# Performance work log

Measured on AMD Instinct MI355X. Metric: run time of the kernel, lower is better.

Reference implementation:

```python
import jax, jax.numpy as jnp
import numpy as np

HIDDEN = 2048
HEADS = 16
HEAD = HIDDEN // HEADS  # 128
MB = 16                 # TTT mini-batch size
LR = 1.0                # inner (test-time) learning rate
ROPE_BASE = 10000.0
LN_EPS = 1e-5


def setup_inputs() -> dict:
    key = jax.random.key(0)
    ks = jax.random.split(key, 7)
    B, S = 4, 2048
    scale = HIDDEN ** -0.5
    x = jax.random.normal(ks[0], (B, S, HIDDEN), jnp.float32)
    Wk = jax.random.normal(ks[1], (HIDDEN, HIDDEN), jnp.float32) * scale
    Wv = jax.random.normal(ks[2], (HIDDEN, HIDDEN), jnp.float32) * scale
    Wo = jax.random.normal(ks[3], (HIDDEN, HIDDEN), jnp.float32) * scale
    ln_g = jnp.ones((HIDDEN,), jnp.float32)
    ln_b = jnp.zeros((HIDDEN,), jnp.float32)
    # initial TTT hidden-state weights, per (batch, head)
    W0 = jax.random.normal(ks[4], (B, HEADS, HEAD, HEAD), jnp.float32) * 0.02
    return {"x": x, "Wk": Wk, "Wv": Wv, "Wo": Wo, "ln_g": ln_g, "ln_b": ln_b, "W0": W0}


def _rotate_half(u):
    u1, u2 = jnp.split(u, 2, axis=-1)
    return jnp.concatenate([-u2, u1], axis=-1)


def _rope(k, seq_len):
    # k: [B, H, S, D]
    inv_freq = 1.0 / (ROPE_BASE ** (jnp.arange(0, HEAD, 2, dtype=jnp.float32) / HEAD))
    t = jnp.arange(seq_len, dtype=jnp.float32)
    freqs = t[:, None] * inv_freq[None, :]          # [S, D/2]
    emb = jnp.concatenate([freqs, freqs], axis=-1)  # [S, D]
    cos, sin = jnp.cos(emb), jnp.sin(emb)
    return k * cos[None, None] + _rotate_half(k) * sin[None, None]


def reference(x, Wk, Wv, Wo, ln_g, ln_b, W0):
    B, S, _ = x.shape
    # projections (nn.Linear convention: y = x @ W.T), split into heads
    k = (x @ Wk.T).reshape(B, S, HEADS, HEAD).transpose(0, 2, 1, 3)  # [B,H,S,D]
    v = (x @ Wv.T).reshape(B, S, HEADS, HEAD).transpose(0, 2, 1, 3)
    k = _rope(k, S)

    nc = S // MB
    # [nc, B, H, MB, D]
    kc = k.reshape(B, HEADS, nc, MB, HEAD).transpose(2, 0, 1, 3, 4)
    vc = v.reshape(B, HEADS, nc, MB, HEAD).transpose(2, 0, 1, 3, 4)

    def step(W, kv):
        k_c, v_c = kv                                   # [B,H,MB,D]
        pred = jnp.einsum('bhmd,bhde->bhme', k_c, W)    # f(k; W) = k W
        err = pred - v_c
        # grad of mean-MSE over (MB*D) elements w.r.t. W: 2/(MB*D) * k^T err
        grad = (2.0 / (MB * HEAD)) * jnp.einsum('bhmd,bhme->bhde', k_c, err)
        W_new = W - LR * grad                           # inner SGD step
        out = jnp.einsum('bhmd,bhde->bhme', k_c, W_new) # output with updated weights
        return W_new, out

    W_final, outs = jax.lax.scan(step, W0, (kc, vc))    # outs: [nc,B,H,MB,D]
    o = outs.transpose(1, 2, 0, 3, 4).reshape(B, HEADS, S, HEAD)
    o = o.transpose(0, 2, 1, 3).reshape(B, S, HIDDEN)

    # LayerNorm + output projection + residual
    mu = o.mean(-1, keepdims=True)
    var = o.var(-1, keepdims=True)
    o = (o - mu) / jnp.sqrt(var + LN_EPS) * ln_g + ln_b
    return x + o @ Wo.T
```

## Files before the change

kernel.cpp:

```cpp
#include <hip/hip_runtime.h>
#include <cstdint>
#include <cstddef>

typedef __attribute__((ext_vector_type(4))) float    f32x4;
typedef __attribute__((ext_vector_type(8))) __bf16   bf16x8;
typedef __attribute__((ext_vector_type(4))) short    s16x4;
typedef __attribute__((ext_vector_type(4))) uint32_t u32x4;
typedef __attribute__((ext_vector_type(2))) uint32_t u32x2;

__device__ __forceinline__ float bf2f(uint16_t h) {
    uint32_t u = ((uint32_t)h) << 16;
    return __builtin_bit_cast(float, u);
}
__device__ __forceinline__ uint16_t f2bf(float f) {
    uint32_t u = __builtin_bit_cast(uint32_t, f);
    uint32_t r = (u + 0x7fffu + ((u >> 16) & 1u)) >> 16;
    return (uint16_t)r;
}
__device__ __forceinline__ uint16_t f2bf_fast(float f) {
    __bf16 h = (__bf16)f;
    return __builtin_bit_cast(uint16_t, h);
}

__device__ __forceinline__ f32x4 mfma32(bf16x8 a, bf16x8 b, f32x4 c) {
    return __builtin_amdgcn_mfma_f32_16x16x32_bf16(a, b, c, 0, 0, 0);
}
__device__ __forceinline__ f32x4 mfma16(s16x4 a, s16x4 b, f32x4 c) {
    return __builtin_amdgcn_mfma_f32_16x16x16bf16_1k(a, b, c, 0, 0, 0);
}

__device__ __forceinline__ void gload16(const void* g, void* l) {
    __builtin_amdgcn_global_load_lds(
        (const __attribute__((address_space(1))) uint32_t*)g,
        (__attribute__((address_space(3))) uint32_t*)l, 16, 0, 0);
}

__global__ __launch_bounds__(256) void cvt_bf16(
    const float* __restrict__ s, uint16_t* __restrict__ d, int n4)
{
    int i = blockIdx.x * 256 + threadIdx.x;
    const int stride = gridDim.x * 256;
    for (; i < n4; i += stride) {
        f32x4 v = ((const f32x4*)s)[i];
        u32x2 p;
        p[0] = (uint32_t)f2bf(v[0]) | ((uint32_t)f2bf(v[1]) << 16);
        p[1] = (uint32_t)f2bf(v[2]) | ((uint32_t)f2bf(v[3]) << 16);
        ((u32x2*)d)[i] = p;
    }
}

template <bool F32OUT>
__global__ __launch_bounds__(512, 2) void gemm256(
    const uint16_t* __restrict__ A, const uint16_t* __restrict__ B,
    void* __restrict__ Cv, const float* __restrict__ R,
    int M, int N, int K)
{
    __shared__ __align__(16) uint16_t lA[2][256 * 64];
    __shared__ __align__(16) uint16_t lB[2][256 * 64];

    const int tid = threadIdx.x;
    const int w = tid >> 6, ln = tid & 63;
    const int l15 = ln & 15, q = ln >> 4;
    const int wm = w >> 2, wn = w & 3;
    const int m0 = blockIdx.y * 256, n0 = blockIdx.x * 256;

    const int srow = w * 32 + (ln >> 3);
    const int scol = ((ln & 7) ^ (ln >> 3)) * 8;
    const uint16_t* gA = A + (size_t)(m0 + srow) * K + scol;
    const uint16_t* gB = B + (size_t)(n0 + srow) * K + scol;

    f32x4 acc[8][4];
    #pragma unroll
    for (int i = 0; i < 8; i++)
        for (int j = 0; j < 4; j++)
            acc[i][j] = (f32x4){0.f, 0.f, 0.f, 0.f};

    const int xs  = (l15 & 7) * 8;
    const int aro = (wm * 128 + l15) * 64;
    const int bro = (wn * 64 + l15) * 64;
    const int k0o = (q * 8) ^ xs;
    const int k1o = (32 + q * 8) ^ xs;

    auto stage = [&](int t) {
        const int s = t & 1;
        const int kt = t * 64;
        #pragma unroll
        for (int i = 0; i < 4; i++)
            gload16(gA + (size_t)(i * 8) * K + kt, lA[s] + (w * 32 + i * 8) * 64);
        #pragma unroll
        for (int i = 0; i < 4; i++)
            gload16(gB + (size_t)(i * 8) * K + kt, lB[s] + (w * 32 + i * 8) * 64);
    };

    const int ntk = K >> 6;
    stage(0);
    __syncthreads();

    for (int t = 0; t < ntk; ++t) {
        const int s = t & 1;
        if (t + 1 < ntk) stage(t + 1);

        const uint16_t* As = lA[s];
        const uint16_t* Bs = lB[s];

        bf16x8 a0[8], b0[4];
        #pragma unroll
        for (int mt = 0; mt < 8; mt++)
            a0[mt] = __builtin_bit_cast(bf16x8,
                *(const u32x4*)(As + aro + mt * 1024 + k0o));
        #pragma unroll
        for (int nt2 = 0; nt2 < 4; nt2++)
            b0[nt2] = __builtin_bit_cast(bf16x8,
                *(const u32x4*)(Bs + bro + nt2 * 1024 + k0o));
        #pragma unroll
        for (int mt = 0; mt < 8; mt++)
            #pragma unroll
            for (int nt2 = 0; nt2 < 4; nt2++)
                acc[mt][nt2] = mfma32(a0[mt], b0[nt2], acc[mt][nt2]);

        bf16x8 a1[8], b1[4];
        #pragma unroll
        for (int mt = 0; mt < 8; mt++)
            a1[mt] = __builtin_bit_cast(bf16x8,
                *(const u32x4*)(As + aro + mt * 1024 + k1o));
        #pragma unroll
        for (int nt2 = 0; nt2 < 4; nt2++)
            b1[nt2] = __builtin_bit_cast(bf16x8,
                *(const u32x4*)(Bs + bro + nt2 * 1024 + k1o));
        #pragma unroll
        for (int mt = 0; mt < 8; mt++)
            #pragma unroll
            for (int nt2 = 0; nt2 < 4; nt2++)
                acc[mt][nt2] = mfma32(a1[mt], b1[nt2], acc[mt][nt2]);

        __syncthreads();
    }

    #pragma unroll
    for (int mt = 0; mt < 8; mt++)
        #pragma unroll
        for (int nt2 = 0; nt2 < 4; nt2++)
            #pragma unroll
            for (int r = 0; r < 4; r++) {
                int row = m0 + wm * 128 + mt * 16 + q * 4 + r;
                int col = n0 + wn * 64 + nt2 * 16 + l15;
                size_t idx = (size_t)row * N + col;
                float v = acc[mt][nt2][r];
                if (F32OUT) {
                    ((float*)Cv)[idx] = v + R[idx];
                } else {
                    ((uint16_t*)Cv)[idx] = f2bf(v);
                }
            }
}

__global__ __launch_bounds__(64) void repack(
    const uint16_t* __restrict__ kb, const uint16_t* __restrict__ vb,
    uint16_t* __restrict__ kp, uint16_t* __restrict__ kt,
    uint16_t* __restrict__ vt)
{
    const int g = blockIdx.x;
    const int c = g & 127, h = (g >> 7) & 15, b = g >> 11;
    const int ln = threadIdx.x;
    const int m = ln >> 2, cb = (ln & 3) * 32;
    const size_t tok = (size_t)b * 2048 + c * 16 + m;
    const int s = c * 16 + m;
    const uint16_t* krow = kb + tok * 2048 + h * 128;
    const uint16_t* vrow = vb + tok * 2048 + h * 128;

    u32x4 kraw[4], praw[4], vraw[4];
    for (int i = 0; i < 4; i++) {
        kraw[i] = *(const u32x4*)(krow + cb + 8 * i);
        praw[i] = *(const u32x4*)(krow + (cb ^ 64) + 8 * i);
        vraw[i] = *(const u32x4*)(vrow + cb + 8 * i);
    }
    const uint16_t* ku = (const uint16_t*)kraw;
    const uint16_t* pu = (const uint16_t*)praw;
    const uint16_t* vu = (const uint16_t*)vraw;

    uint16_t ko[32];
    for (int j = 0; j < 32; j++) {
        int col = cb + j;
        int p = col & 63;
        float invf = exp2f((float)p * (-13.287712379549449f / 64.0f));
        float a = (float)s * invf;
        float sn, cs;
        __sincosf(a, &sn, &cs);
        float u1 = bf2f(ku[j]), u2 = bf2f(pu[j]);
        float o = (col < 64) ? (u1 * cs - u2 * sn) : (u1 * cs + u2 * sn);
        ko[j] = f2bf(o);
    }

    uint16_t* kpg = kp + (size_t)g * 2048;
    uint16_t* ktg = kt + (size_t)g * 2048;
    uint16_t* vtg = vt + (size_t)g * 2048;
    for (int i = 0; i < 4; i++) {
        u32x4 pk;
        uint32_t* pw = (uint32_t*)&pk;
        for (int w = 0; w < 4; w++)
            pw[w] = (uint32_t)ko[8 * i + 2 * w] | ((uint32_t)ko[8 * i + 2 * w + 1] << 16);
        *(u32x4*)(kpg + m * 128 + cb + 8 * i) = pk;
    }
    for (int j = 0; j < 32; j++) {
        ktg[(cb + j) * 16 + m] = ko[j];
        vtg[(cb + j) * 16 + m] = vu[j];
    }
}

__global__ __launch_bounds__(64, 1) void ttt_scan(
    const uint16_t* __restrict__ kp, const uint16_t* __restrict__ kt,
    const uint16_t* __restrict__ vt, const float* __restrict__ W0,
    uint16_t* __restrict__ O)
{
    const int bid = blockIdx.x;
    const int g  = bid & 63;
    const int e0 = (bid >> 6) * 16;
    const int h = g & 15, b = g >> 4;
    const int ln = threadIdx.x;
    const int l15 = ln & 15, q = ln >> 4;

    f32x4 W[8];
    s16x4 Wb[8];
    {
        const float* w0p = W0 + (size_t)g * 128 * 128;
        #pragma unroll
        for (int mt = 0; mt < 8; mt++)
            for (int r = 0; r < 4; r++)
                W[mt][r] = w0p[(size_t)(16 * mt + 4 * q + r) * 128 + e0 + l15];
    }
    #pragma unroll
    for (int mt = 0; mt < 8; mt++)
        for (int r = 0; r < 4; r++)
            Wb[mt][r] = (short)f2bf_fast(W[mt][r]);

    const uint16_t* kpw = kp + (size_t)g * 128 * 2048;
    const uint16_t* ktw = kt + (size_t)g * 128 * 2048;
    const uint16_t* vtw = vt + (size_t)g * 128 * 2048;
    uint16_t*     obase = O  + (size_t)b * 2048 * 2048 + h * 128 + e0;

    auto loadset = [&](int c, u32x2* ka, u32x2* ktf, u32x2* vv) {
        const uint16_t* kc = kpw + (size_t)c * 2048;
        const uint16_t* tc = ktw + (size_t)c * 2048;
        const uint16_t* vc = vtw + (size_t)c * 2048;
        #pragma unroll
        for (int dt = 0; dt < 8; dt++)
            ka[dt] = *(const u32x2*)(kc + l15 * 128 + 16 * dt + 4 * q);
        #pragma unroll
        for (int mt = 0; mt < 8; mt++)
            ktf[mt] = *(const u32x2*)(tc + (16 * mt + l15) * 16 + 4 * q);
        vv[0] = *(const u32x2*)(vc + (e0 + l15) * 16 + 4 * q);
    };

    auto step = [&](int c, const u32x2* ka, const u32x2* ktf, const u32x2* vv) {
        const int s0 = c * 16;

        f32x4 pA = (f32x4){0.f, 0.f, 0.f, 0.f};
        f32x4 pB = (f32x4){0.f, 0.f, 0.f, 0.f};
        f32x4 gA = (f32x4){0.f, 0.f, 0.f, 0.f};
        f32x4 gB = (f32x4){0.f, 0.f, 0.f, 0.f};
        #pragma unroll
        for (int dt = 0; dt < 8; dt++) {
            s16x4 kf = __builtin_bit_cast(s16x4, ka[dt]);
            if (dt & 1) { pB = mfma16(kf, Wb[dt], pB); gB = mfma16(kf, kf, gB); }
            else        { pA = mfma16(kf, Wb[dt], pA); gA = mfma16(kf, kf, gA); }
        }
        f32x4 p, gacc;
        #pragma unroll
        for (int r = 0; r < 4; r++) { p[r] = pA[r] + pB[r]; gacc[r] = gA[r] + gB[r]; }

        s16x4 vvs = __builtin_bit_cast(s16x4, vv[0]);
        s16x4 es, gf;
        #pragma unroll
        for (int r = 0; r < 4; r++) {
            es[r] = (short)f2bf_fast((bf2f((uint16_t)vvs[r]) - p[r]) * (1.0f / 1024.0f));
            gf[r] = (short)f2bf_fast(gacc[r]);
        }

        f32x4 o = mfma16(gf, es, p);

        #pragma unroll
        for (int mt = 0; mt < 8; mt++) {
            s16x4 kf = __builtin_bit_cast(s16x4, ktf[mt]);
            W[mt] = mfma16(kf, es, W[mt]);
            #pragma unroll
            for (int r = 0; r < 4; r++)
                Wb[mt][r] = (short)f2bf_fast(W[mt][r]);
        }

        #pragma unroll
        for (int r = 0; r < 4; r++)
            obase[(size_t)(s0 + 4 * q + r) * 2048 + l15] = f2bf_fast(o[r]);
    };

    u32x2 kaA[8], kaB[8];
    u32x2 ktA[8], ktB[8];
    u32x2 vvA[1], vvB[1];
    loadset(0, kaA, ktA, vvA);
    loadset(1, kaB, ktB, vvB);

    for (int c = 0; c < 128; c += 2) {
        step(c, kaA, ktA, vvA);
        if (c < 126) loadset(c + 2, kaA, ktA, vvA);
        step(c + 1, kaB, ktB, vvB);
        if (c < 126) loadset(c + 3, kaB, ktB, vvB);
    }
}

__global__ __launch_bounds__(256) void ln_kernel(
    const uint16_t* __restrict__ X, const float* __restrict__ Gm,
    const float* __restrict__ Bt, uint16_t* __restrict__ Y)
{
    const int row = blockIdx.x, t = threadIdx.x;
    const uint16_t* xr = X + (size_t)row * 2048 + t * 8;
    u32x4 raw = *(const u32x4*)xr;
    const uint16_t* pr = (const uint16_t*)&raw;
    float v[8];
    float s = 0.f, s2 = 0.f;
    for (int i = 0; i < 8; i++) {
        v[i] = bf2f(pr[i]);
        s += v[i];
        s2 += v[i] * v[i];
    }
    for (int off = 32; off; off >>= 1) {
        s  += __shfl_down(s, off, 64);
        s2 += __shfl_down(s2, off, 64);
    }
    __shared__ float red[8];
    if ((t & 63) == 0) { red[(t >> 6) * 2] = s; red[(t >> 6) * 2 + 1] = s2; }
    __syncthreads();
    float ts  = red[0] + red[2] + red[4] + red[6];
    float ts2 = red[1] + red[3] + red[5] + red[7];
    float mu  = ts * (1.0f / 2048.0f);
    float var = ts2 * (1.0f / 2048.0f) - mu * mu;
    float inv = rsqrtf(var + 1e-5f);
    uint16_t outv[8];
    for (int i = 0; i < 8; i++) {
        float y = (v[i] - mu) * inv * Gm[t * 8 + i] + Bt[t * 8 + i];
        outv[i] = f2bf(y);
    }
    u32x4 ov;
    __builtin_memcpy(&ov, outv, 16);
    *(u32x4*)(Y + (size_t)row * 2048 + t * 8) = ov;
}

extern "C" void kernel_launch(void* const* d_in, const int* in_sizes, int n_in,
                              void* d_out, int out_size, void* d_ws, size_t ws_size,
                              hipStream_t stream)
{
    const float* x  = (const float*)d_in[0];
    const float* Wk = (const float*)d_in[1];
    const float* Wv = (const float*)d_in[2];
    const float* Wo = (const float*)d_in[3];
    const float* lg = (const float*)d_in[4];
    const float* lb = (const float*)d_in[5];
    const float* W0 = (const float*)d_in[6];
    float* out = (float*)d_out;

    const size_t NTOK = 8192, HID = 2048;
    uint16_t* xb   = (uint16_t*)d_ws;
    uint16_t* wbuf = xb + NTOK * HID;
    uint16_t* kb   = wbuf + HID * HID;
    uint16_t* vb   = kb + NTOK * HID;
    uint16_t* kt   = vb + NTOK * HID;
    uint16_t* vt   = kt + NTOK * HID;
    uint16_t* kp   = xb;
    uint16_t* ob   = (uint16_t*)d_out;
    uint16_t* lnb  = kb;

    dim3 grid(8, 32), blk(512);
    const int nX4 = (int)(NTOK * HID / 4), nW4 = (int)(HID * HID / 4);

    cvt_bf16<<<4096, 256, 0, stream>>>(x, xb, nX4);
    cvt_bf16<<<4096, 256, 0, stream>>>(Wk, wbuf, nW4);
    gemm256<false><<<grid, blk, 0, stream>>>(xb, wbuf, kb, nullptr, 8192, 2048, 2048);
    cvt_bf16<<<4096, 256, 0, stream>>>(Wv, wbuf, nW4);
    gemm256<false><<<grid, blk, 0, stream>>>(xb, wbuf, vb, nullptr, 8192, 2048, 2048);
    repack<<<8192, 64, 0, stream>>>(kb, vb, kp, kt, vt);
    ttt_scan<<<512, 64, 0, stream>>>(kp, kt, vt, W0, ob);
    ln_kernel<<<8192, 256, 0, stream>>>(ob, lg, lb, lnb);
    cvt_bf16<<<4096, 256, 0, stream>>>(Wo, wbuf, nW4);
    gemm256<true><<<grid, blk, 0, stream>>>(lnb, wbuf, out, x, 8192, 2048, 2048);
}
```

Before: 541.2 us.

## Split GEMM K-tile staging into half-tiles and interleave loads with MFMA phases

Restructures the 256x256 GEMM main loop so each 64-wide K tile is loaded as four 128-row half-tiles. Those loads are issued between eight MFMA phases per two K tiles, and explicit s_waitcnt vmcnt plus s_barrier replace the per-tile __syncthreads. MFMA blocks are wrapped in s_setprio to favour math issue. The intent is to overlap global-to-LDS transfers with compute more finely and cut barrier stalls. In exchange, the hand-counted vmcnt values and barrier placement must match the load ordering exactly. The loop also assumes K is a multiple of 128.

```diff
diff --git a/kernel.cpp b/kernel.cpp
--- a/kernel.cpp
+++ b/kernel.cpp
@@ -55,8 +55,8 @@
     void* __restrict__ Cv, const float* __restrict__ R,
     int M, int N, int K)
 {
-    __shared__ __align__(16) uint16_t lA[2][256 * 64];
-    __shared__ __align__(16) uint16_t lB[2][256 * 64];
+    __shared__ __align__(16) uint16_t lA[2][2][128 * 64];
+    __shared__ __align__(16) uint16_t lB[2][2][128 * 64];
 
     const int tid = threadIdx.x;
     const int w = tid >> 6, ln = tid & 63;
@@ -64,10 +64,10 @@
     const int wm = w >> 2, wn = w & 3;
     const int m0 = blockIdx.y * 256, n0 = blockIdx.x * 256;
 
-    const int srow = w * 32 + (ln >> 3);
-    const int scol = ((ln & 7) ^ (ln >> 3)) * 8;
-    const uint16_t* gA = A + (size_t)(m0 + srow) * K + scol;
-    const uint16_t* gB = B + (size_t)(n0 + srow) * K + scol;
+    const int srow8 = ln >> 3;
+    const int scol  = ((ln & 7) ^ srow8) * 8;
+    const uint16_t* gA = A + (size_t)(m0 + w * 8 + srow8) * K + scol;
+    const uint16_t* gB = B + (size_t)(n0 + w * 8 + srow8) * K + scol;
 
     f32x4 acc[8][4];
     #pragma unroll
@@ -75,65 +75,77 @@
         for (int j = 0; j < 4; j++)
             acc[i][j] = (f32x4){0.f, 0.f, 0.f, 0.f};
 
-    const int xs  = (l15 & 7) * 8;
-    const int aro = (wm * 128 + l15) * 64;
-    const int bro = (wn * 64 + l15) * 64;
-    const int k0o = (q * 8) ^ xs;
-    const int k1o = (32 + q * 8) ^ xs;
-
-    auto stage = [&](int t) {
-        const int s = t & 1;
+    const int axr = (l15 & 7) * 8;
+
+    auto stage_half = [&](int t, int h) {
+        const int slot = t & 1;
         const int kt = t * 64;
-        #pragma unroll
-        for (int i = 0; i < 4; i++)
-            gload16(gA + (size_t)(i * 8) * K + kt, lA[s] + (w * 32 + i * 8) * 64);
-        #pragma unroll
-        for (int i = 0; i < 4; i++)
-            gload16(gB + (size_t)(i * 8) * K + kt, lB[s] + (w * 32 + i * 8) * 64);
+        if (h < 2) {
+            const uint16_t* g = gA + (size_t)(h * 128) * K + kt;
+            uint16_t* l = &lA[slot][h][(w * 8) * 64];
+            gload16(g,                  l);
+            gload16(g + (size_t)64 * K, l + 64 * 64);
+        } else {
+            const int hh = h - 2;
+            const uint16_t* g = gB + (size_t)(hh * 128) * K + kt;
+            uint16_t* l = &lB[slot][hh][(w * 8) * 64];
+            gload16(g,                  l);
+            gload16(g + (size_t)64 * K, l + 64 * 64);
+        }
     };
 
-    const int ntk = K >> 6;
-    stage(0);
-    __syncthreads();
-
-    for (int t = 0; t < ntk; ++t) {
-        const int s = t & 1;
-        if (t + 1 < ntk) stage(t + 1);
-
-        const uint16_t* As = lA[s];
-        const uint16_t* Bs = lB[s];
-
-        bf16x8 a0[8], b0[4];
-        #pragma unroll
-        for (int mt = 0; mt < 8; mt++)
-            a0[mt] = __builtin_bit_cast(bf16x8,
-                *(const u32x4*)(As + aro + mt * 1024 + k0o));
-        #pragma unroll
-        for (int nt2 = 0; nt2 < 4; nt2++)
-            b0[nt2] = __builtin_bit_cast(bf16x8,
-                *(const u32x4*)(Bs + bro + nt2 * 1024 + k0o));
-        #pragma unroll
-        for (int mt = 0; mt < 8; mt++)
-            #pragma unroll
-            for (int nt2 = 0; nt2 < 4; nt2++)
-                acc[mt][nt2] = mfma32(a0[mt], b0[nt2], acc[mt][nt2]);
-
-        bf16x8 a1[8], b1[4];
-        #pragma unroll
-        for (int mt = 0; mt < 8; mt++)
-            a1[mt] = __builtin_bit_cast(bf16x8,
-                *(const u32x4*)(As + aro + mt * 1024 + k1o));
-        #pragma unroll
-        for (int nt2 = 0; nt2 < 4; nt2++)
-            b1[nt2] = __builtin_bit_cast(bf16x8,
-                *(const u32x4*)(Bs + bro + nt2 * 1024 + k1o));
-        #pragma unroll
-        for (int mt = 0; mt < 8; mt++)
-            #pragma unroll
-            for (int nt2 = 0; nt2 < 4; nt2++)
-                acc[mt][nt2] = mfma32(a1[mt], b1[nt2], acc[mt][nt2]);
-
-        __syncthreads();
+    stage_half(0, 0); stage_half(0, 1); stage_half(0, 2); stage_half(0, 3);
+
+    const int L = K >> 7;
+
+    for (int i = 0; i < L; ++i) {
+        const int tN1 = 2 * i + 1;
+        const int tN2 = 2 * i + 2;
+        const bool last = (i == L - 1);
+
+        #pragma unroll
+        for (int p = 0; p < 8; ++p) {
+            const int slot_r = p >> 2;
+            const int qm = p & 1, qk = (p >> 1) & 1;
+            const int h = p & 3;
+
+            if (p < 4)      stage_half(tN1, h);
+            else if (!last) stage_half(tN2, h);
+
+            if (p == 0) {
+                asm volatile("s_waitcnt vmcnt(2)\n\ts_barrier" ::: "memory");
+            } else if (p == 4) {
+                if (last) asm volatile("s_waitcnt vmcnt(0)\n\ts_barrier" ::: "memory");
+                else      asm volatile("s_waitcnt vmcnt(2)\n\ts_barrier" ::: "memory");
+            }
+
+            const int ko = (qk * 32 + q * 8) ^ axr;
+            bf16x8 af[4], bfv[4];
+            #pragma unroll
+            for (int mtl = 0; mtl < 4; ++mtl) {
+                const int rowin = (qm * 4 + mtl) * 16 + l15;
+                af[mtl] = __builtin_bit_cast(bf16x8,
+                    *(const u32x4*)&lA[slot_r][wm][rowin * 64 + ko]);
+            }
+            #pragma unroll
+            for (int nt = 0; nt < 4; ++nt) {
+                const int rowin = (wn & 1) * 64 + nt * 16 + l15;
+                bfv[nt] = __builtin_bit_cast(bf16x8,
+                    *(const u32x4*)&lB[slot_r][wn >> 1][rowin * 64 + ko]);
+            }
+
+            __builtin_amdgcn_s_setprio(1);
+            #pragma unroll
+            for (int mtl = 0; mtl < 4; ++mtl)
+                #pragma unroll
+                for (int nt = 0; nt < 4; ++nt)
+                    acc[qm * 4 + mtl][nt] =
+                        mfma32(af[mtl], bfv[nt], acc[qm * 4 + mtl][nt]);
+            __builtin_amdgcn_s_setprio(0);
+
+            if (p == 3 || p == 7)
+                asm volatile("s_barrier" ::: "memory");
+        }
     }
 
     #pragma unroll
```

New measurement: 554.8 us. 1.03x slower.
